# Kernel optimization log

Hardware: AMD Instinct MI355X
Metric: run time of the kernel (lower is better)

The kernel has to match this reference:

```python
import jax, jax.numpy as jnp
import numpy as np

HQ, HKV, HD = 8, 4, 256          # query heads, kv heads, head dim
SW = 1024                         # sliding window (layer_idx=0 is even -> window active)
EPS = 1e-6
SCALE = 256.0 ** -0.5             # query_pre_attn_scalar ** -0.5
THETA = 10000.0
NEG = jnp.finfo(jnp.float32).min


def _rms_norm(x, w):
    # Gemma2 RMSNorm: fp32 variance, weight applied as (1 + kernel)
    var = jnp.mean(jnp.square(x.astype(jnp.float32)), axis=-1, keepdims=True)
    xn = x / jnp.sqrt(var + EPS)
    return (1.0 + w) * xn


def _rope(q, k, positions):
    # standard rotate-half RoPE over full head_dim
    inv = 1.0 / (THETA ** (jnp.arange(0, HD, 2, dtype=jnp.float32) / HD))  # [HD/2]
    freqs = positions.astype(jnp.float32)[..., None] * inv                  # [B,S,HD/2]
    emb = jnp.concatenate([freqs, freqs], axis=-1)                          # [B,S,HD]
    cos = jnp.cos(emb)[:, :, None, :]
    sin = jnp.sin(emb)[:, :, None, :]
    def rot(x):
        return jnp.concatenate([-x[..., HD // 2:], x[..., :HD // 2]], axis=-1)
    return q * cos + rot(q) * sin, k * cos + rot(k) * sin


def setup_inputs() -> dict:
    key = jax.random.key(0)
    ks = jax.random.split(key, 12)
    B, S, D, I = 1, 2048, 2304, 9216
    std = 0.02
    return {
        "hidden_states": jax.random.normal(ks[0], (B, S, D), jnp.float32),
        "attention_mask": jnp.ones((B, S), jnp.int32),
        "position_ids": jnp.broadcast_to(jnp.arange(S, dtype=jnp.int32)[None], (B, S)),
        "wq": jax.random.normal(ks[1], (D, HQ * HD), jnp.float32) * std,
        "wk": jax.random.normal(ks[2], (D, HKV * HD), jnp.float32) * std,
        "wv": jax.random.normal(ks[3], (D, HKV * HD), jnp.float32) * std,
        "wo": jax.random.normal(ks[4], (HQ * HD, D), jnp.float32) * std,
        "w_gate": jax.random.normal(ks[5], (D, I), jnp.float32) * std,
        "w_up": jax.random.normal(ks[6], (D, I), jnp.float32) * std,
        "w_down": jax.random.normal(ks[7], (I, D), jnp.float32) * std,
        "ln_in": jax.random.uniform(ks[8], (D,), jnp.float32) * 0.1,
        "ln_post_attn": jax.random.uniform(ks[9], (D,), jnp.float32) * 0.1,
        "ln_pre_ffn": jax.random.uniform(ks[10], (D,), jnp.float32) * 0.1,
        "ln_post_ffn": jax.random.uniform(ks[11], (D,), jnp.float32) * 0.1,
    }


def _attention(h, attention_mask, position_ids, wq, wk, wv, wo):
    B, S, _ = h.shape
    q = (h @ wq).reshape(B, S, HQ, HD)
    k = (h @ wk).reshape(B, S, HKV, HD)
    v = (h @ wv).reshape(B, S, HKV, HD)
    q, k = _rope(q, k, position_ids)
    # GQA: repeat kv heads
    groups = HQ // HKV
    k = jnp.repeat(k, groups, axis=2)  # [B,S,HQ,HD]
    v = jnp.repeat(v, groups, axis=2)
    # combined mask: causal AND within sliding window AND padding mask
    i = jnp.arange(S)[:, None]
    j = jnp.arange(S)[None, :]
    keep = (j <= i) & ((i - j) < SW)                       # [S,S]
    keep = keep[None, None] & (attention_mask[:, None, None, :] > 0)  # [B,1,S,S]
    bias = jnp.where(keep, 0.0, NEG).astype(jnp.float32)
    scores = jnp.einsum("bqhd,bkhd->bhqk", q, k) * SCALE + bias
    probs = jax.nn.softmax(scores, axis=-1)
    out = jnp.einsum("bhqk,bkhd->bqhd", probs, v).reshape(B, S, HQ * HD)
    return out @ wo


def reference(hidden_states, attention_mask, position_ids, wq, wk, wv, wo,
              w_gate, w_up, w_down, ln_in, ln_post_attn, ln_pre_ffn, ln_post_ffn):
    # Gemma2 decoder layer with sandwich norms
    residual = hidden_states
    h = _rms_norm(hidden_states, ln_in)
    attn = _attention(h, attention_mask, position_ids, wq, wk, wv, wo)
    h = _rms_norm(attn, ln_post_attn)
    x = residual + h
    residual = x
    h = _rms_norm(x, ln_pre_ffn)
    h = (jax.nn.gelu(h @ w_gate, approximate=True) * (h @ w_up)) @ w_down
    h = _rms_norm(h, ln_post_ffn)
    return residual + h
```

## Files before the change

kernel.cpp:

```cpp
#include <hip/hip_runtime.h>
#include <stdint.h>
#include <type_traits>

typedef unsigned short u16;
typedef unsigned int u32;
typedef __bf16 bf16x8 __attribute__((ext_vector_type(8)));
typedef float f32x4 __attribute__((ext_vector_type(4)));

#define S_LEN 2048
#define DMODEL 2304
#define DFF 9216
#define NHQ 8
#define NHKV 4
#define HDIM 256
#define SWIN 1024

template <int N> using IC = std::integral_constant<int, N>;

__device__ __forceinline__ u16 f2bf(float f) {
  u32 u = __float_as_uint(f);
  u = (u + 0x7FFFu + ((u >> 16) & 1)) >> 16;
  return (u16)u;
}
__device__ __forceinline__ float bf2f(u16 h) {
  return __uint_as_float(((u32)h) << 16);
}

__device__ __forceinline__ void gload_lds16(const void* g, void* l) {
  __builtin_amdgcn_global_load_lds((const __attribute__((address_space(1))) u32*)g,
                                   (__attribute__((address_space(3))) u32*)l, 16, 0, 0);
}

template <int N>
__device__ __forceinline__ void wait_vmcnt() {
  if constexpr (N == 0) asm volatile("s_waitcnt vmcnt(0)" ::: "memory");
  else if constexpr (N == 4) asm volatile("s_waitcnt vmcnt(4)" ::: "memory");
  else if constexpr (N == 5) asm volatile("s_waitcnt vmcnt(5)" ::: "memory");
  else if constexpr (N == 6) asm volatile("s_waitcnt vmcnt(6)" ::: "memory");
  else if constexpr (N == 8) asm volatile("s_waitcnt vmcnt(8)" ::: "memory");
}

__device__ __forceinline__ float gelu_t(float x) {
  float u = 0.7978845608f * (x + 0.044715f * x * x * x);
  float e = __expf(2.f * u);
  float t = 1.f - 2.f / (e + 1.f);
  return 0.5f * x * (1.f + t);
}

__global__ __launch_bounds__(256) void transpose_convert(
    const float* __restrict__ in, u16* __restrict__ out, int K, int N, int stride) {
  __shared__ float t[32][130];
  const int k0 = blockIdx.x * 32, n0 = blockIdx.y * 128;
  const int tx = threadIdx.x & 31, ty = threadIdx.x >> 5;
#pragma unroll
  for (int r = 0; r < 4; ++r) {
    const float4 v = *(const float4*)&in[(size_t)(k0 + ty + r * 8) * stride + n0 + 4 * tx];
    t[ty + r * 8][4 * tx + 0] = v.x;
    t[ty + r * 8][4 * tx + 1] = v.y;
    t[ty + r * 8][4 * tx + 2] = v.z;
    t[ty + r * 8][4 * tx + 3] = v.w;
  }
  __syncthreads();
  const int kk = threadIdx.x & 15, nn = threadIdx.x >> 4;
#pragma unroll
  for (int r = 0; r < 8; ++r) {
    const int n = nn + r * 16;
    const u32 p = (u32)f2bf(t[2 * kk][n]) | ((u32)f2bf(t[2 * kk + 1][n]) << 16);
    *(u32*)&out[(size_t)(n0 + n) * K + k0 + 2 * kk] = p;
  }
}

__global__ __launch_bounds__(256) void transpose_qkv_kernel(
    const float* __restrict__ wq, const float* __restrict__ wk,
    const float* __restrict__ wv, u16* __restrict__ out) {
  const int k0 = blockIdx.x * 32;
  const int n0g = blockIdx.y * 128;
  const float* in; int n0, N;
  if (n0g < 2048)      { in = wq; n0 = n0g;        N = 2048; }
  else if (n0g < 3072) { in = wk; n0 = n0g - 2048; N = 1024; }
  else                 { in = wv; n0 = n0g - 3072; N = 1024; }
  __shared__ float t[32][130];
  const int tx = threadIdx.x & 31, ty = threadIdx.x >> 5;
#pragma unroll
  for (int r = 0; r < 4; ++r) {
    const float4 v = *(const float4*)&in[(size_t)(k0 + ty + r * 8) * N + n0 + 4 * tx];
    t[ty + r * 8][4 * tx + 0] = v.x;
    t[ty + r * 8][4 * tx + 1] = v.y;
    t[ty + r * 8][4 * tx + 2] = v.z;
    t[ty + r * 8][4 * tx + 3] = v.w;
  }
  __syncthreads();
  const int kk = threadIdx.x & 15, nn = threadIdx.x >> 4;
#pragma unroll
  for (int r = 0; r < 8; ++r) {
    const int n = nn + r * 16;
    const u32 p = (u32)f2bf(t[2 * kk][n]) | ((u32)f2bf(t[2 * kk + 1][n]) << 16);
    *(u32*)&out[(size_t)(n0g + n) * DMODEL + k0 + 2 * kk] = p;
  }
}

__global__ __launch_bounds__(256) void vpack_kernel(
    const float* __restrict__ qkvf, u16* __restrict__ vtile) {
  __shared__ float t[32][33];
  const int s0 = blockIdx.x * 32, d0 = blockIdx.y * 32, kvh = blockIdx.z;
  const int tx = threadIdx.x & 31, ty = threadIdx.x >> 5;
#pragma unroll
  for (int r = 0; r < 4; ++r)
    t[ty + r * 8][tx] = qkvf[(size_t)(s0 + ty + r * 8) * 4096 + 3072 + kvh * HDIM + d0 + tx];
  __syncthreads();
  const int kk = threadIdx.x & 15, nn = threadIdx.x >> 4;
#pragma unroll
  for (int r = 0; r < 2; ++r) {
    const int d = nn + r * 16;
    const u32 p = (u32)f2bf(t[2 * kk][d]) | ((u32)f2bf(t[2 * kk + 1][d]) << 16);
    *(u32*)&vtile[(((size_t)kvh * 64 + (s0 >> 5)) * 256 + d0 + d) * 32 + 2 * kk] = p;
  }
}

__device__ __forceinline__ float block_sumsq(const float* xr, int D) {
  float ss = 0.f;
  for (int d = threadIdx.x; d < D; d += 256) { float v = xr[d]; ss += v * v; }
#pragma unroll
  for (int m = 1; m < 64; m <<= 1) ss += __shfl_xor(ss, m, 64);
  __shared__ float red[4];
  if ((threadIdx.x & 63) == 0) red[threadIdx.x >> 6] = ss;
  __syncthreads();
  return red[0] + red[1] + red[2] + red[3];
}

__global__ __launch_bounds__(256) void rmsnorm_bf16_kernel(
    const float* __restrict__ x, const float* __restrict__ w, u16* __restrict__ o) {
  const int row = blockIdx.x;
  const float* xr = x + (size_t)row * DMODEL;
  float tot = block_sumsq(xr, DMODEL);
  float inv = rsqrtf(tot / DMODEL + 1e-6f);
  u16* orow = o + (size_t)row * DMODEL;
  for (int d = threadIdx.x; d < DMODEL; d += 256)
    orow[d] = f2bf((1.f + w[d]) * (xr[d] * inv));
}

__global__ __launch_bounds__(256) void rms_add_rms_kernel(
    const u16* __restrict__ p, const float* __restrict__ w1,
    const float* __restrict__ res, const float* __restrict__ w2,
    float* __restrict__ xres, u16* __restrict__ hn) {
  const int row = blockIdx.x;
  const size_t PS = (size_t)S_LEN * DMODEL;
  const u16* pr = p + (size_t)row * DMODEL;
  const float* rr = res + (size_t)row * DMODEL;
  __shared__ float red[2][4];
  float yv[9];
  float ss = 0.f;
#pragma unroll
  for (int e = 0; e < 9; ++e) {
    const int d = threadIdx.x + e * 256;
    float v = 0.f;
#pragma unroll
    for (int k = 0; k < 4; ++k) v += bf2f(pr[d + k * PS]);
    yv[e] = v;
    ss += v * v;
  }
#pragma unroll
  for (int m = 1; m < 64; m <<= 1) ss += __shfl_xor(ss, m, 64);
  if ((threadIdx.x & 63) == 0) red[0][threadIdx.x >> 6] = ss;
  __syncthreads();
  const float inv1 = rsqrtf((red[0][0] + red[0][1] + red[0][2] + red[0][3]) / DMODEL + 1e-6f);
  float* xr = xres + (size_t)row * DMODEL;
  float xv[9];
  float ss2 = 0.f;
#pragma unroll
  for (int e = 0; e < 9; ++e) {
    const int d = threadIdx.x + e * 256;
    float x = rr[d] + (1.f + w1[d]) * (yv[e] * inv1);
    xv[e] = x;
    xr[d] = x;
    ss2 += x * x;
  }
#pragma unroll
  for (int m = 1; m < 64; m <<= 1) ss2 += __shfl_xor(ss2, m, 64);
  if ((threadIdx.x & 63) == 0) red[1][threadIdx.x >> 6] = ss2;
  __syncthreads();
  const float inv2 = rsqrtf((red[1][0] + red[1][1] + red[1][2] + red[1][3]) / DMODEL + 1e-6f);
  u16* hr = hn + (size_t)row * DMODEL;
#pragma unroll
  for (int e = 0; e < 9; ++e) {
    const int d = threadIdx.x + e * 256;
    hr[d] = f2bf((1.f + w2[d]) * (xv[e] * inv2));
  }
}

__global__ __launch_bounds__(256) void reduce8_rms_add_kernel(
    const u16* __restrict__ p, const float* __restrict__ w,
    const float* __restrict__ res, float* __restrict__ o) {
  const int row = blockIdx.x;
  const size_t PS = (size_t)S_LEN * DMODEL;
  const u16* pr = p + (size_t)row * DMODEL;
  float y[9];
  float ss = 0.f;
#pragma unroll
  for (int e = 0; e < 9; ++e) {
    const int d = threadIdx.x + e * 256;
    float v = 0.f;
#pragma unroll
    for (int k = 0; k < 8; ++k) v += bf2f(pr[d + k * PS]);
    y[e] = v;
    ss += v * v;
  }
#pragma unroll
  for (int m = 1; m < 64; m <<= 1) ss += __shfl_xor(ss, m, 64);
  __shared__ float red[4];
  if ((threadIdx.x & 63) == 0) red[threadIdx.x >> 6] = ss;
  __syncthreads();
  const float tot = red[0] + red[1] + red[2] + red[3];
  const float inv = rsqrtf(tot / DMODEL + 1e-6f);
  const float* rr = res + (size_t)row * DMODEL;
  float* orow = o + (size_t)row * DMODEL;
#pragma unroll
  for (int e = 0; e < 9; ++e) {
    const int d = threadIdx.x + e * 256;
    orow[d] = rr[d] + (1.f + w[d]) * (y[e] * inv);
  }
}

__global__ void rope_kernel(const float* __restrict__ qkv, const int* __restrict__ pos,
                            u16* __restrict__ qb, u16* __restrict__ kt) {
  const int s = blockIdx.x;
  const int t = threadIdx.x;
  float p = (float)pos[s];
  float inv = powf(10000.f, -(float)(2 * t) / (float)HDIM);
  float f = p * inv;
  float cs = cosf(f), sn = sinf(f);
  const float* row = qkv + (size_t)s * 4096;
  u16* qr = qb + (size_t)s * (NHQ * HDIM);
#pragma unroll
  for (int h = 0; h < NHQ; ++h) {
    float x1 = row[h * HDIM + t], x2 = row[h * HDIM + t + 128];
    qr[h * HDIM + t] = f2bf(x1 * cs - x2 * sn);
    qr[h * HDIM + t + 128] = f2bf(x2 * cs + x1 * sn);
  }
#pragma unroll
  for (int h = 0; h < NHKV; ++h) {
    u16* kr = kt + ((size_t)h * S_LEN + s) * HDIM;
    float x1 = row[2048 + h * HDIM + t], x2 = row[2048 + h * HDIM + t + 128];
    kr[t] = f2bf(x1 * cs - x2 * sn);
    kr[t + 128] = f2bf(x2 * cs + x1 * sn);
  }
}

template <int BN, int MODE, int BUFS>
__global__ __launch_bounds__(512) void gemm_pipe(
    const u16* __restrict__ A, const u16* __restrict__ Bt, const u16* __restrict__ Bt2,
    void* __restrict__ Cv, void* __restrict__ Cv2,
    int M, int N, int Klen, int LDK, int ntn, int n1,
    const u16* __restrict__ gptr) {
  constexpr bool DUAL = (MODE == 4);
  constexpr int CH_B = BN / 8;
  constexpr int CH_TOT = 16 + (DUAL ? 2 * CH_B : CH_B);
  constexpr int LPW = CH_TOT / 8;
  constexpr int TILE = CH_TOT * 512;
  constexpr int NFR = BN / 64;
  __shared__ __align__(16) u16 smem[BUFS * TILE];

  const int tid = threadIdx.x;
  const int lane = tid & 63, wave = tid >> 6;
  const int wr = wave >> 2, wc = wave & 3;
  const int l15 = lane & 15, l16 = lane >> 4;

  const int MB = M >> 7;
  const int nwg = gridDim.x;
  const int orig = blockIdx.x;
  const int q = nwg >> 3, r = nwg & 7, xcd = orig & 7, lidx = orig >> 3;
  const int wg = (xcd < r ? xcd * (q + 1) : r * (q + 1) + (xcd - r) * q) + lidx;
  const int tiles = MB * ntn;
  const int kz = wg / tiles, wgt = wg % tiles;
  const int bm = wgt % MB, bn = wgt / MB;
  const bool side2 = !DUAL && bn >= n1;
  const int bnl = side2 ? bn - n1 : bn;
  const u16* Bp = side2 ? Bt2 : Bt;

  const u16* Az = A + (size_t)kz * Klen;
  const u16* Bz = Bp + (size_t)kz * Klen;
  const int NT = Klen >> 6;

  const u16* src[LPW];
  const int swz = (((lane & 7) ^ (lane >> 3)) * 8);
#pragma unroll
  for (int i = 0; i < LPW; ++i) {
    const int c = wave * LPW + i;
    if (c < 16) src[i] = Az + (size_t)(bm * 128 + c * 8 + (lane >> 3)) * LDK + swz;
    else if (!DUAL || c < 16 + CH_B)
      src[i] = Bz + (size_t)(bnl * BN + (c - 16) * 8 + (lane >> 3)) * LDK + swz;
    else
      src[i] = Bt2 + (size_t)kz * Klen + (size_t)(bnl * BN + (c - 16 - CH_B) * 8 + (lane >> 3)) * LDK + swz;
  }
  const int dst0 = wave * LPW * 512 + lane * 8;

  auto STAGE = [&](int buf, int kt) {
    u16* base = smem + buf * TILE + dst0;
    const size_t ko = (size_t)kt * 64;
#pragma unroll
    for (int i = 0; i < LPW; ++i) gload_lds16(src[i] + ko, base + i * 512);
  };

  f32x4 acc[4][NFR];
  f32x4 acc2[DUAL ? 4 : 1][DUAL ? NFR : 1];
#pragma unroll
  for (int m = 0; m < 4; ++m)
#pragma unroll
    for (int n = 0; n < NFR; ++n) {
      acc[m][n] = f32x4{0.f, 0.f, 0.f, 0.f};
      if constexpr (DUAL) acc2[m][n] = f32x4{0.f, 0.f, 0.f, 0.f};
    }

  auto COMPUTE = [&](int buf) {
    const u16* Ab = smem + buf * TILE;
    const u16* Bb = Ab + 16 * 512;
    const u16* Ub = Ab + (16 + CH_B) * 512;
    bf16x8 a[2][4], b[2][NFR];
    bf16x8 u[DUAL ? 2 : 1][DUAL ? NFR : 1];
#pragma unroll
    for (int kk = 0; kk < 2; ++kk) {
      const int cc = kk * 4 + l16;
#pragma unroll
      for (int m = 0; m < 4; ++m) {
        const int rr = wr * 64 + m * 16 + l15;
        a[kk][m] = *(const bf16x8*)&Ab[rr * 64 + ((cc ^ (rr & 7)) * 8)];
      }
#pragma unroll
      for (int n = 0; n < NFR; ++n) {
        const int rr = wc * (BN / 4) + n * 16 + l15;
        b[kk][n] = *(const bf16x8*)&Bb[rr * 64 + ((cc ^ (rr & 7)) * 8)];
        if constexpr (DUAL)
          u[kk][n] = *(const bf16x8*)&Ub[rr * 64 + ((cc ^ (rr & 7)) * 8)];
      }
    }
    __builtin_amdgcn_s_setprio(1);
#pragma unroll
    for (int kk = 0; kk < 2; ++kk)
#pragma unroll
      for (int m = 0; m < 4; ++m)
#pragma unroll
        for (int n = 0; n < NFR; ++n)
          acc[m][n] = __builtin_amdgcn_mfma_f32_16x16x32_bf16(a[kk][m], b[kk][n], acc[m][n], 0, 0, 0);
    if constexpr (DUAL) {
#pragma unroll
      for (int kk = 0; kk < 2; ++kk)
#pragma unroll
        for (int m = 0; m < 4; ++m)
#pragma unroll
          for (int n = 0; n < NFR; ++n)
            acc2[m][n] = __builtin_amdgcn_mfma_f32_16x16x32_bf16(a[kk][m], u[kk][n], acc2[m][n], 0, 0, 0);
    }
    __builtin_amdgcn_s_setprio(0);
  };

  if constexpr (BUFS == 2) {
    STAGE(0, 0);
    wait_vmcnt<0>();
    __builtin_amdgcn_s_barrier();
    int cur = 0;
    for (int t = 0; t < NT; ++t) {
      if (t + 1 < NT) STAGE(cur ^ 1, t + 1);
      COMPUTE(cur);
      if (t + 1 < NT) { wait_vmcnt<0>(); __builtin_amdgcn_s_barrier(); }
      cur ^= 1;
    }
  } else {
    STAGE(0, 0);
    STAGE(1, 1);
    wait_vmcnt<LPW>();
    __builtin_amdgcn_s_barrier();
    int cur = 0;
    for (int t = 0; t < NT; ++t) {
      const int nb = (cur >= 1) ? cur - 1 : cur + 2;
      if (t + 2 < NT) STAGE(nb, t + 2);
      COMPUTE(cur);
      if (t + 1 < NT) {
        if (t + 2 < NT) wait_vmcnt<LPW>();
        else            wait_vmcnt<0>();
        __builtin_amdgcn_s_barrier();
      }
      cur = (cur == 2) ? 0 : cur + 1;
    }
  }

  const int row0 = bm * 128 + wr * 64 + l16 * 4;
  const int col0 = bnl * BN + wc * (BN / 4) + l15;
  float* Cf = (float*)(side2 ? Cv2 : Cv) + (size_t)kz * M * N;
  u16* Cb = (u16*)(side2 ? Cv2 : Cv) + (size_t)kz * M * N;
#pragma unroll
  for (int m = 0; m < 4; ++m)
#pragma unroll
    for (int n = 0; n < NFR; ++n)
#pragma unroll
      for (int rr = 0; rr < 4; ++rr) {
        const size_t idx = (size_t)(row0 + m * 16 + rr) * N + col0 + n * 16;
        if (MODE == 0) Cf[idx] = acc[m][n][rr];
        else if (MODE == 1) Cb[idx] = f2bf(acc[m][n][rr]);
        else if (MODE == 2) ((u16*)Cv)[idx] = f2bf(gelu_t(bf2f(gptr[idx])) * acc[m][n][rr]);
        else if (MODE == 4) {
          if constexpr (DUAL)
            ((u16*)Cv)[idx] = f2bf(gelu_t(acc[m][n][rr]) * acc2[m][n][rr]);
        }
      }
}

__global__ __launch_bounds__(256) void attn_kernel(
    const u16* __restrict__ qb, const u16* __restrict__ kt,
    const u16* __restrict__ vtile, const int* __restrict__ amask,
    u16* __restrict__ outp) {
  __shared__ __align__(16) u16 Ks[2][32 * 256];
  __shared__ __align__(16) u16 Vs[2][256 * 32];
  __shared__ __align__(16) u16 Ps[4][16 * 40];
  const int bid = blockIdx.x;
  const int qh = bid & 7;
  const int qblk = bid >> 3;
  const int kvh = qh >> 1;
  const int q0 = qblk * 64;
  const int tid = threadIdx.x, lane = tid & 63, wave = tid >> 6;
  const int qrow = q0 + wave * 16;
  const int l15 = lane & 15, l16 = lane >> 4;

  bf16x8 qf[8];
  {
    const u16* qp = qb + (size_t)(qrow + l15) * (NHQ * HDIM) + qh * HDIM + l16 * 8;
#pragma unroll
    for (int kc = 0; kc < 8; ++kc) qf[kc] = *(const bf16x8*)(qp + kc * 32);
  }
  f32x4 acc[16];
#pragma unroll
  for (int n = 0; n < 16; ++n) acc[n] = f32x4{0.f, 0.f, 0.f, 0.f};
  float mr[4] = {-1e30f, -1e30f, -1e30f, -1e30f};
  float sr[4] = {0.f, 0.f, 0.f, 0.f};

  int lo = q0 - (SWIN - 1); if (lo < 0) lo = 0; lo &= ~31;
  const int ntiles = ((q0 + 63 - lo) >> 5) + 1;

  const char* kbase = (const char*)(kt + (size_t)kvh * S_LEN * HDIM);
  const char* vbase = (const char*)(vtile + (size_t)kvh * 64 * 256 * 32);

  auto STAGEKV = [&](int buf, int key0) {
    const char* ksrc = kbase + (size_t)key0 * 512;
    const char* vsrc = vbase + (size_t)(key0 >> 5) * 16384;
#pragma unroll
    for (int i = 0; i < 4; ++i) {
      const int b = (wave * 4 + i) * 1024 + lane * 16;
      gload_lds16(ksrc + (b ^ (((b >> 9) & 7) << 4)), (char*)&Ks[buf][0] + (wave * 4 + i) * 1024);
    }
#pragma unroll
    for (int i = 0; i < 4; ++i) {
      const int b = (wave * 4 + i) * 1024 + lane * 16;
      gload_lds16(vsrc + (b ^ (((b >> 6) & 3) << 4)), (char*)&Vs[buf][0] + (wave * 4 + i) * 1024);
    }
  };

  STAGEKV(0, lo);
  wait_vmcnt<0>();
  __builtin_amdgcn_s_barrier();

  int cur = 0;
  for (int it = 0; it < ntiles; ++it) {
    const int key0 = lo + it * 32;
    const int am0 = amask[key0 + l15];
    const int am1 = amask[key0 + 16 + l15];
    if (it + 1 < ntiles) { STAGEKV(cur ^ 1, key0 + 32); wait_vmcnt<8>(); }
    else                 { wait_vmcnt<0>(); }
    __builtin_amdgcn_s_barrier();

    if (key0 <= qrow + 15 && key0 + 31 >= qrow - (SWIN - 1)) {
      f32x4 sc[2];
      sc[0] = f32x4{0.f, 0.f, 0.f, 0.f};
      sc[1] = f32x4{0.f, 0.f, 0.f, 0.f};
#pragma unroll
      for (int ct = 0; ct < 2; ++ct) {
        const int r = ct * 16 + l15;
#pragma unroll
        for (int kc = 0; kc < 8; ++kc) {
          const int byte = (r * 512 + kc * 64 + l16 * 16) ^ ((r & 7) << 4);
          bf16x8 kf = *(const bf16x8*)((const char*)&Ks[cur][0] + byte);
          sc[ct] = __builtin_amdgcn_mfma_f32_16x16x32_bf16(qf[kc], kf, sc[ct], 0, 0, 0);
        }
      }
      float pr[2][4];
#pragma unroll
      for (int ct = 0; ct < 2; ++ct) {
        const int j = key0 + ct * 16 + l15;
        const bool jok = (ct ? am1 : am0) > 0;
#pragma unroll
        for (int r = 0; r < 4; ++r) {
          const int i = qrow + l16 * 4 + r;
          const bool ok = jok && (j <= i) && (i - j < SWIN);
          pr[ct][r] = ok ? sc[ct][r] * 0.0625f : -1e30f;
        }
      }
      float resc[4];
#pragma unroll
      for (int r = 0; r < 4; ++r) {
        float mx = fmaxf(pr[0][r], pr[1][r]);
#pragma unroll
        for (int mm = 1; mm < 16; mm <<= 1) mx = fmaxf(mx, __shfl_xor(mx, mm, 64));
        const float mnew = fmaxf(mr[r], mx);
        const float rs = __expf(mr[r] - mnew);
        mr[r] = mnew;
        float p0 = __expf(pr[0][r] - mnew);
        float p1 = __expf(pr[1][r] - mnew);
        pr[0][r] = p0; pr[1][r] = p1;
        float sm = p0 + p1;
#pragma unroll
        for (int mm = 1; mm < 16; mm <<= 1) sm += __shfl_xor(sm, mm, 64);
        sr[r] = sr[r] * rs + sm;
        resc[r] = rs;
      }
#pragma unroll
      for (int n = 0; n < 16; ++n)
#pragma unroll
        for (int r = 0; r < 4; ++r) acc[n][r] *= resc[r];
      u16* P = &Ps[wave][0];
#pragma unroll
      for (int ct = 0; ct < 2; ++ct)
#pragma unroll
        for (int r = 0; r < 4; ++r)
          P[(l16 * 4 + r) * 40 + ct * 16 + l15] = f2bf(pr[ct][r]);
      bf16x8 pa = *(const bf16x8*)&P[l15 * 40 + l16 * 8];
#pragma unroll
      for (int n = 0; n < 16; ++n) {
        const int d = n * 16 + l15;
        const int byte = (d * 64 + l16 * 16) ^ ((d & 3) << 4);
        bf16x8 vf = *(const bf16x8*)((const char*)&Vs[cur][0] + byte);
        acc[n] = __builtin_amdgcn_mfma_f32_16x16x32_bf16(pa, vf, acc[n], 0, 0, 0);
      }
    }
    __builtin_amdgcn_s_barrier();
    cur ^= 1;
  }
#pragma unroll
  for (int n = 0; n < 16; ++n)
#pragma unroll
    for (int r = 0; r < 4; ++r) {
      const int i = qrow + l16 * 4 + r;
      outp[(size_t)i * (NHQ * HDIM) + qh * HDIM + n * 16 + l15] = f2bf(acc[n][r] / sr[r]);
    }
}

__global__ void gelu_mul_kernel(const u16* __restrict__ g, const u16* __restrict__ u,
                                u16* __restrict__ o, int n8) {
  const int idx0 = blockIdx.x * blockDim.x + threadIdx.x;
  const int stride = gridDim.x * blockDim.x;
  for (int i = idx0; i < n8; i += stride) {
    uint4 gv = ((const uint4*)g)[i];
    uint4 uv = ((const uint4*)u)[i];
    u32 gg[4] = {gv.x, gv.y, gv.z, gv.w};
    u32 uu[4] = {uv.x, uv.y, uv.z, uv.w};
    u32 ow[4];
#pragma unroll
    for (int w = 0; w < 4; ++w) {
      float x0 = bf2f((u16)(gg[w] & 0xffff)), x1 = bf2f((u16)(gg[w] >> 16));
      float y0 = bf2f((u16)(uu[w] & 0xffff)), y1 = bf2f((u16)(uu[w] >> 16));
      ow[w] = (u32)f2bf(gelu_t(x0) * y0) | ((u32)f2bf(gelu_t(x1) * y1) << 16);
    }
    ((uint4*)o)[i] = make_uint4(ow[0], ow[1], ow[2], ow[3]);
  }
}

extern "C" void kernel_launch(void* const* d_in, const int* in_sizes, int n_in,
                              void* d_out, int out_size, void* d_ws, size_t ws_size,
                              hipStream_t stream) {
  const float* hidden = (const float*)d_in[0];
  const int*   amask  = (const int*)d_in[1];
  const int*   pos    = (const int*)d_in[2];
  const float* wq     = (const float*)d_in[3];
  const float* wk     = (const float*)d_in[4];
  const float* wv     = (const float*)d_in[5];
  const float* wo     = (const float*)d_in[6];
  const float* wg     = (const float*)d_in[7];
  const float* wu     = (const float*)d_in[8];
  const float* wd     = (const float*)d_in[9];
  const float* ln_in  = (const float*)d_in[10];
  const float* ln_pa  = (const float*)d_in[11];
  const float* ln_pf  = (const float*)d_in[12];
  const float* ln_po  = (const float*)d_in[13];
  float* out = (float*)d_out;

  char* ws = (char*)d_ws;
  size_t off = 0;
  auto alloc = [&](size_t b) { char* p = ws + off; off += (b + 255) & ~(size_t)255; return p; };
  u16*   WT    = (u16*)alloc((size_t)DFF * DMODEL * 2);
  u16*   hnorm = (u16*)alloc((size_t)S_LEN * DMODEL * 2);
  char*  big0  = alloc((size_t)S_LEN * DFF * 2);
  u16*   qb    = (u16*)alloc((size_t)S_LEN * NHQ * HDIM * 2);
  u16*   ktb   = (u16*)alloc((size_t)NHKV * S_LEN * HDIM * 2);
  u16*   vtile = (u16*)alloc((size_t)NHKV * 64 * 256 * 32 * 2);
  u16*   attn  = (u16*)alloc((size_t)S_LEN * NHQ * HDIM * 2);
  float* f32t  = (float*)alloc((size_t)S_LEN * DMODEL * 4);
  float* xres  = (float*)alloc((size_t)S_LEN * DMODEL * 4);
  u16*   gbuf  = (u16*)alloc((size_t)S_LEN * DFF * 2);
  u16*   ubuf  = (u16*)alloc((size_t)S_LEN * DFF * 2);
  u16*   WTU   = (u16*)alloc((size_t)DFF * DMODEL * 2);
  const bool fused_gu = (off <= ws_size);
  (void)n_in; (void)in_sizes; (void)out_size; (void)f32t; (void)ubuf;
  float* qkvf = (float*)big0;
  u16*   ggu  = (u16*)big0;
  u16*   opart = (u16*)big0;
  u16*   part = gbuf;
  const size_t PS = (size_t)S_LEN * DMODEL;
  (void)PS;

  const dim3 B256(256), B128(128), B512(512);

  rmsnorm_bf16_kernel<<<dim3(S_LEN), B256, 0, stream>>>(hidden, ln_in, hnorm);
  transpose_qkv_kernel<<<dim3(DMODEL / 32, 4096 / 128), B256, 0, stream>>>(wq, wk, wv, WT);
  gemm_pipe<128, 0, 2><<<dim3(512), B512, 0, stream>>>(hnorm, WT, WT, qkvf, qkvf, S_LEN, 4096, DMODEL, DMODEL, 32, 32, nullptr);
  rope_kernel<<<dim3(S_LEN), B128, 0, stream>>>(qkvf, pos, qb, ktb);
  vpack_kernel<<<dim3(S_LEN / 32, HDIM / 32, NHKV), B256, 0, stream>>>(qkvf, vtile);
  attn_kernel<<<dim3((S_LEN / 64) * NHQ), B256, 0, stream>>>(qb, ktb, vtile, amask, attn);
  transpose_convert<<<dim3(2048 / 32, DMODEL / 128), B256, 0, stream>>>(wo, WT, 2048, DMODEL, DMODEL);
  gemm_pipe<192, 1, 2><<<dim3(768), B512, 0, stream>>>(attn, WT, WT, opart, opart, S_LEN, DMODEL, 512, 2048, 12, 12, nullptr);
  rms_add_rms_kernel<<<dim3(S_LEN), B256, 0, stream>>>(opart, ln_pa, hidden, ln_pf, xres, hnorm);
  if (fused_gu) {
    transpose_convert<<<dim3(DMODEL / 32, DFF / 128), B256, 0, stream>>>(wg, WT, DMODEL, DFF, DFF);
    transpose_convert<<<dim3(DMODEL / 32, DFF / 128), B256, 0, stream>>>(wu, WTU, DMODEL, DFF, DFF);
    gemm_pipe<192, 4, 2><<<dim3(768), B512, 0, stream>>>(hnorm, WT, WTU, ggu, nullptr, S_LEN, DFF, DMODEL, DMODEL, 48, 48, nullptr);
  } else {
    transpose_convert<<<dim3(DMODEL / 32, DFF / 128), B256, 0, stream>>>(wg, WT, DMODEL, DFF, DFF);
    gemm_pipe<192, 1, 3><<<dim3(768), B512, 0, stream>>>(hnorm, WT, WT, gbuf, gbuf, S_LEN, DFF, DMODEL, DMODEL, 48, 48, nullptr);
    transpose_convert<<<dim3(DMODEL / 32, DFF / 128), B256, 0, stream>>>(wu, WT, DMODEL, DFF, DFF);
    gemm_pipe<192, 2, 3><<<dim3(768), B512, 0, stream>>>(hnorm, WT, WT, ggu, ggu, S_LEN, DFF, DMODEL, DMODEL, 48, 48, gbuf);
  }
  transpose_convert<<<dim3(DFF / 32, DMODEL / 128), B256, 0, stream>>>(wd, WT, DFF, DMODEL, DMODEL);
  gemm_pipe<192, 1, 2><<<dim3(1536), B512, 0, stream>>>(ggu, WT, WT, part, part, S_LEN, DMODEL, DFF / 8, DFF, 12, 12, nullptr);
  reduce8_rms_add_kernel<<<dim3(S_LEN), B256, 0, stream>>>(part, ln_po, xres, out);
}
```

Before: 578.0 us.

## Run fused gate/up GEMM with 64-row tiles, 4 waves, single-buffered LDS

The gemm_pipe template gains parameters for the M-tile height and the wave count, plus a single-buffer mode that stages and computes without overlap. The fused gate/up GEMM now launches with 64x192 tiles, 4 waves (256 threads), one LDS buffer and twice as many workgroups. The aim is to cut LDS use and per-block resources so more blocks fit per CU and occupancy rises for the register-heavy dual-accumulator kernel. The cost is losing the double-buffered load/compute overlap, adding more barriers per K step, and re-reading the B tiles twice as often.

Result: slower. 637.0 us (+10.2%).

```diff
diff --git a/kernel.cpp b/kernel.cpp
--- a/kernel.cpp
+++ b/kernel.cpp
@@ -246,26 +246,28 @@
   }
 }
 
-template <int BN, int MODE, int BUFS>
-__global__ __launch_bounds__(512) void gemm_pipe(
+template <int BN, int MODE, int BUFS, int BMT = 128, int NW = 8>
+__global__ __launch_bounds__(NW * 64) void gemm_pipe(
     const u16* __restrict__ A, const u16* __restrict__ Bt, const u16* __restrict__ Bt2,
     void* __restrict__ Cv, void* __restrict__ Cv2,
     int M, int N, int Klen, int LDK, int ntn, int n1,
     const u16* __restrict__ gptr) {
   constexpr bool DUAL = (MODE == 4);
+  constexpr int CH_A = BMT / 8;
   constexpr int CH_B = BN / 8;
-  constexpr int CH_TOT = 16 + (DUAL ? 2 * CH_B : CH_B);
-  constexpr int LPW = CH_TOT / 8;
+  constexpr int CH_TOT = CH_A + (DUAL ? 2 * CH_B : CH_B);
+  constexpr int LPW = CH_TOT / NW;
   constexpr int TILE = CH_TOT * 512;
   constexpr int NFR = BN / 64;
   __shared__ __align__(16) u16 smem[BUFS * TILE];
 
   const int tid = threadIdx.x;
   const int lane = tid & 63, wave = tid >> 6;
-  const int wr = wave >> 2, wc = wave & 3;
+  const int wr = (NW == 8) ? (wave >> 2) : 0;
+  const int wc = (NW == 8) ? (wave & 3) : wave;
   const int l15 = lane & 15, l16 = lane >> 4;
 
-  const int MB = M >> 7;
+  const int MB = M / BMT;
   const int nwg = gridDim.x;
   const int orig = blockIdx.x;
   const int q = nwg >> 3, r = nwg & 7, xcd = orig & 7, lidx = orig >> 3;
@@ -286,11 +288,11 @@
 #pragma unroll
   for (int i = 0; i < LPW; ++i) {
     const int c = wave * LPW + i;
-    if (c < 16) src[i] = Az + (size_t)(bm * 128 + c * 8 + (lane >> 3)) * LDK + swz;
-    else if (!DUAL || c < 16 + CH_B)
-      src[i] = Bz + (size_t)(bnl * BN + (c - 16) * 8 + (lane >> 3)) * LDK + swz;
+    if (c < CH_A) src[i] = Az + (size_t)(bm * BMT + c * 8 + (lane >> 3)) * LDK + swz;
+    else if (!DUAL || c < CH_A + CH_B)
+      src[i] = Bz + (size_t)(bnl * BN + (c - CH_A) * 8 + (lane >> 3)) * LDK + swz;
     else
-      src[i] = Bt2 + (size_t)kz * Klen + (size_t)(bnl * BN + (c - 16 - CH_B) * 8 + (lane >> 3)) * LDK + swz;
+      src[i] = Bt2 + (size_t)kz * Klen + (size_t)(bnl * BN + (c - CH_A - CH_B) * 8 + (lane >> 3)) * LDK + swz;
   }
   const int dst0 = wave * LPW * 512 + lane * 8;
 
@@ -313,8 +315,8 @@
 
   auto COMPUTE = [&](int buf) {
     const u16* Ab = smem + buf * TILE;
-    const u16* Bb = Ab + 16 * 512;
-    const u16* Ub = Ab + (16 + CH_B) * 512;
+    const u16* Bb = Ab + CH_A * 512;
+    const u16* Ub = Ab + (CH_A + CH_B) * 512;
     bf16x8 a[2][4], b[2][NFR];
     bf16x8 u[DUAL ? 2 : 1][DUAL ? NFR : 1];
 #pragma unroll
@@ -353,7 +355,15 @@
     __builtin_amdgcn_s_setprio(0);
   };
 
-  if constexpr (BUFS == 2) {
+  if constexpr (BUFS == 1) {
+    for (int t = 0; t < NT; ++t) {
+      STAGE(0, t);
+      wait_vmcnt<0>();
+      __builtin_amdgcn_s_barrier();
+      COMPUTE(0);
+      __builtin_amdgcn_s_barrier();
+    }
+  } else if constexpr (BUFS == 2) {
     STAGE(0, 0);
     wait_vmcnt<0>();
     __builtin_amdgcn_s_barrier();
@@ -383,7 +393,7 @@
     }
   }
 
-  const int row0 = bm * 128 + wr * 64 + l16 * 4;
+  const int row0 = bm * BMT + wr * 64 + l16 * 4;
   const int col0 = bnl * BN + wc * (BN / 4) + l15;
   float* Cf = (float*)(side2 ? Cv2 : Cv) + (size_t)kz * M * N;
   u16* Cb = (u16*)(side2 ? Cv2 : Cv) + (size_t)kz * M * N;
@@ -618,7 +628,7 @@
   if (fused_gu) {
     transpose_convert<<<dim3(DMODEL / 32, DFF / 128), B256, 0, stream>>>(wg, WT, DMODEL, DFF, DFF);
     transpose_convert<<<dim3(DMODEL / 32, DFF / 128), B256, 0, stream>>>(wu, WTU, DMODEL, DFF, DFF);
-    gemm_pipe<192, 4, 2><<<dim3(768), B512, 0, stream>>>(hnorm, WT, WTU, ggu, nullptr, S_LEN, DFF, DMODEL, DMODEL, 48, 48, nullptr);
+    gemm_pipe<192, 4, 1, 64, 4><<<dim3(1536), B256, 0, stream>>>(hnorm, WT, WTU, ggu, nullptr, S_LEN, DFF, DMODEL, DMODEL, 48, 48, nullptr);
   } else {
     transpose_convert<<<dim3(DMODEL / 32, DFF / 128), B256, 0, stream>>>(wg, WT, DMODEL, DFF, DFF);
     gemm_pipe<192, 1, 3><<<dim3(768), B512, 0, stream>>>(hnorm, WT, WT, gbuf, gbuf, S_LEN, DFF, DMODEL, DMODEL, 48, 48, nullptr);
```
